# Kernel tuning notes

Measured on AMD Instinct MI355X. Metric: run time of the kernel, lower is better.

## Reference

```python
import jax, jax.numpy as jnp
import numpy as np

DIM = 576
NUM_HEADS = 1
HEAD_DIM = DIM // NUM_HEADS
SCALE = HEAD_DIM ** -0.5


def layer_norm(x, w, b, eps=1e-5):
    mu = jnp.mean(x, axis=-1, keepdims=True)
    var = jnp.var(x, axis=-1, keepdims=True)
    return (x - mu) * jax.lax.rsqrt(var + eps) * w + b


def setup_inputs() -> dict:
    key = jax.random.key(0)
    ks = jax.random.split(key, 10)
    B, N, C = 8, 2048, DIM
    s = C ** -0.5
    return {
        "x": jax.random.normal(ks[0], (B, N, C), jnp.float32),
        "y": jax.random.normal(ks[1], (B, N, C), jnp.float32),
        "Wq": jax.random.normal(ks[2], (C, C), jnp.float32) * s,
        "Wk": jax.random.normal(ks[3], (C, C), jnp.float32) * s,
        "Wv": jax.random.normal(ks[4], (C, C), jnp.float32) * s,
        "Wp": jax.random.normal(ks[5], (C, C), jnp.float32) * s,
        "bp": jnp.zeros((C,), jnp.float32),
        "gx": jnp.ones((C,), jnp.float32), "bx": jnp.zeros((C,), jnp.float32),
        "gy": jnp.ones((C,), jnp.float32), "by": jnp.zeros((C,), jnp.float32),
        "gz": jnp.ones((C,), jnp.float32), "bz": jnp.zeros((C,), jnp.float32),
    }


def reference(x, y, Wq, Wk, Wv, Wp, bp, gx, bx, gy, by, gz, bz):
    B, N, C = x.shape
    H, D = NUM_HEADS, HEAD_DIM
    xn = layer_norm(x, gx, bx)
    yn = layer_norm(y, gy, by)
    # torch Linear: out = in @ W^T
    q = (yn @ Wq.T).reshape(B, N, H, D).transpose(0, 2, 1, 3)  # [B,H,N,D]
    k = (xn @ Wk.T).reshape(B, N, H, D).transpose(0, 2, 1, 3)
    v = (xn @ Wv.T).reshape(B, N, H, D).transpose(0, 2, 1, 3)
    attn = jax.nn.sigmoid(jnp.einsum("bhnd,bhmd->bhnm", q, k) * SCALE)
    out = jnp.einsum("bhnm,bhmd->bhnd", attn, v).transpose(0, 2, 1, 3).reshape(B, N, C)
    out = out @ Wp.T + bp
    out = out + xn  # residual with normalized x
    return layer_norm(out, gz, bz)
```

## Files before the change

kernel.cpp:

```cpp
#include <hip/hip_runtime.h>

typedef __bf16 bfrag __attribute__((ext_vector_type(8)));
typedef float f32x4 __attribute__((ext_vector_type(4)));

__device__ __forceinline__ unsigned short f2bf(float f) {
    unsigned int u = __float_as_uint(f);
    unsigned int r = (u + 0x7fffu + ((u >> 16) & 1u)) >> 16;
    return (unsigned short)r;
}
__device__ __forceinline__ float bf2f(unsigned short h) {
    return __uint_as_float(((unsigned int)h) << 16);
}

__device__ __forceinline__ void gll16(const unsigned short* g, unsigned short* l) {
    __builtin_amdgcn_global_load_lds(
        (const __attribute__((address_space(1))) unsigned int*)g,
        (__attribute__((address_space(3))) unsigned int*)l, 16, 0, 0);
}

__device__ __forceinline__ float fsigmoid(float v) {
    return __builtin_amdgcn_rcpf(1.0f + __expf(-v));
}

__device__ __forceinline__ int swz(int r, int kc) {
    return (r >> 3) * 512 + (((r & 7) * 8 + (kc ^ (r & 7))) * 8);
}

template<int BM, int BN, int WR, int WC, int EPI, int TM, int TN, int N, int K>
__global__ __launch_bounds__(256) void gemm_nt(
    const unsigned short* __restrict__ A, const unsigned short* __restrict__ B,
    unsigned short* __restrict__ Cb,
    const unsigned short* __restrict__ R, const float* __restrict__ bias,
    float scale, size_t sAz, size_t sBz, size_t sCz)
{
    constexpr int BK = 64;
    constexpr int WTM = BM / (WR * 16);
    constexpr int WTN = BN / (WC * 16);
    constexpr int NA = BM / 32, NB = BN / 32;
    __shared__ unsigned short sA[BM * BK];
    __shared__ unsigned short sB[BN * BK];

    const int id  = blockIdx.x;
    const int j   = id >> 3;
    const int s   = (id & 7) + 8 * (j / TN);
    const int bn0 = (j % TN) * BN;
    const int bm0 = (s % TM) * BM;
    const int z   = s / TM;

    A += (size_t)z * sAz;
    B += (size_t)z * sBz;

    const int tid  = threadIdx.x;
    const int w    = tid >> 6;
    const int lane = tid & 63;
    const int wm = w / WC;
    const int wn = w % WC;
    const int rl  = lane >> 3;
    const int kcs = (lane & 7) ^ rl;
    const int mrow = lane & 15;
    const int kgrp = lane >> 4;

    const unsigned short* pA[NA];
    const unsigned short* pB[NB];
    #pragma unroll
    for (int i = 0; i < NA; ++i) {
        int wc = w * NA + i;
        pA[i] = A + (size_t)(bm0 + wc * 8 + rl) * K + kcs * 8;
    }
    #pragma unroll
    for (int i = 0; i < NB; ++i) {
        int wc = w * NB + i;
        pB[i] = B + (size_t)(bn0 + wc * 8 + rl) * K + kcs * 8;
    }

    f32x4 acc[WTM][WTN] = {};

    for (int k0 = 0; k0 < K; k0 += BK) {
        #pragma unroll
        for (int i = 0; i < NA; ++i) {
            gll16(pA[i], &sA[(w * NA + i) * 512 + lane * 8]);
            pA[i] += BK;
        }
        #pragma unroll
        for (int i = 0; i < NB; ++i) {
            gll16(pB[i], &sB[(w * NB + i) * 512 + lane * 8]);
            pB[i] += BK;
        }
        __syncthreads();

        #pragma unroll
        for (int kh = 0; kh < 2; ++kh) {
            bfrag af[WTM], bfr[WTN];
            #pragma unroll
            for (int mt = 0; mt < WTM; ++mt)
                af[mt] = *(const bfrag*)&sA[swz(wm * WTM * 16 + mt * 16 + mrow, kh * 4 + kgrp)];
            #pragma unroll
            for (int nt = 0; nt < WTN; ++nt)
                bfr[nt] = *(const bfrag*)&sB[swz(wn * WTN * 16 + nt * 16 + mrow, kh * 4 + kgrp)];
            #pragma unroll
            for (int mt = 0; mt < WTM; ++mt)
                #pragma unroll
                for (int nt = 0; nt < WTN; ++nt)
                    acc[mt][nt] = __builtin_amdgcn_mfma_f32_16x16x32_bf16(af[mt], bfr[nt], acc[mt][nt], 0, 0, 0);
        }
        __syncthreads();
    }

    #pragma unroll
    for (int mt = 0; mt < WTM; ++mt) {
        #pragma unroll
        for (int nt = 0; nt < WTN; ++nt) {
            int grow0 = bm0 + wm * WTM * 16 + mt * 16 + kgrp * 4;
            int gcol  = bn0 + wn * WTN * 16 + nt * 16 + mrow;
            #pragma unroll
            for (int r = 0; r < 4; ++r) {
                float v = acc[mt][nt][r];
                size_t off = (size_t)z * sCz + (size_t)(grow0 + r) * N + gcol;
                if (EPI == 0) {
                    Cb[off] = f2bf(v * scale);
                } else if (EPI == 1) {
                    Cb[off] = f2bf(fsigmoid(v));
                } else {
                    Cb[off] = f2bf(v + bias[gcol] + bf2f(R[off]));
                }
            }
        }
    }
}

__global__ __launch_bounds__(256) void qkv_proj(
    const unsigned short* __restrict__ xn, const unsigned short* __restrict__ yn,
    const unsigned short* __restrict__ W,
    unsigned short* __restrict__ qk,
    unsigned short* __restrict__ vt,
    float scale)
{
    constexpr int BM = 128, BN = 64, BK = 64;
    constexpr int WTM = 4, WTN = 2;
    constexpr int NA = 4, NB = 2;
    __shared__ unsigned short sA[BM * BK];
    __shared__ unsigned short sB[BN * BK];

    const int id  = blockIdx.x;
    const int j   = id >> 3;
    const int s   = (id & 7) + 8 * (j / 9);
    const int bn0 = (j % 9) * BN;
    const int bm0 = (s % 128) * BM;
    const int z   = s / 128;

    const unsigned short* A = (z == 0) ? yn : xn;
    const unsigned short* B = W + (size_t)z * 576 * 576;
    const float sc = (z == 0) ? scale : 1.0f;

    const int tid  = threadIdx.x;
    const int w    = tid >> 6;
    const int lane = tid & 63;
    const int wm = w >> 1;
    const int wn = w & 1;
    const int rl  = lane >> 3;
    const int kcs = (lane & 7) ^ rl;
    const int mrow = lane & 15;
    const int kgrp = lane >> 4;

    const unsigned short* pA[NA];
    const unsigned short* pB[NB];
    #pragma unroll
    for (int i = 0; i < NA; ++i) {
        int wc = w * NA + i;
        pA[i] = A + (size_t)(bm0 + wc * 8 + rl) * 576 + kcs * 8;
    }
    #pragma unroll
    for (int i = 0; i < NB; ++i) {
        int wc = w * NB + i;
        pB[i] = B + (size_t)(bn0 + wc * 8 + rl) * 576 + kcs * 8;
    }

    f32x4 acc[WTM][WTN] = {};

    for (int k0 = 0; k0 < 576; k0 += BK) {
        #pragma unroll
        for (int i = 0; i < NA; ++i) {
            gll16(pA[i], &sA[(w * NA + i) * 512 + lane * 8]);
            pA[i] += BK;
        }
        #pragma unroll
        for (int i = 0; i < NB; ++i) {
            gll16(pB[i], &sB[(w * NB + i) * 512 + lane * 8]);
            pB[i] += BK;
        }
        __syncthreads();

        #pragma unroll
        for (int kh = 0; kh < 2; ++kh) {
            bfrag af[WTM], bfr[WTN];
            #pragma unroll
            for (int mt = 0; mt < WTM; ++mt)
                af[mt] = *(const bfrag*)&sA[swz(wm * WTM * 16 + mt * 16 + mrow, kh * 4 + kgrp)];
            #pragma unroll
            for (int nt = 0; nt < WTN; ++nt)
                bfr[nt] = *(const bfrag*)&sB[swz(wn * WTN * 16 + nt * 16 + mrow, kh * 4 + kgrp)];
            #pragma unroll
            for (int mt = 0; mt < WTM; ++mt)
                #pragma unroll
                for (int nt = 0; nt < WTN; ++nt)
                    acc[mt][nt] = __builtin_amdgcn_mfma_f32_16x16x32_bf16(af[mt], bfr[nt], acc[mt][nt], 0, 0, 0);
        }
        __syncthreads();
    }

    #pragma unroll
    for (int mt = 0; mt < WTM; ++mt) {
        #pragma unroll
        for (int nt = 0; nt < WTN; ++nt) {
            int grow0 = bm0 + wm * WTM * 16 + mt * 16 + kgrp * 4;
            int gcol  = bn0 + wn * WTN * 16 + nt * 16 + mrow;
            if (z == 2) {
                ushort4 o;
                o.x = f2bf(acc[mt][nt][0]);
                o.y = f2bf(acc[mt][nt][1]);
                o.z = f2bf(acc[mt][nt][2]);
                o.w = f2bf(acc[mt][nt][3]);
                size_t dst = (((size_t)(grow0 >> 11) * 576 + gcol) << 11) + (grow0 & 2047);
                *(ushort4*)(vt + dst) = o;
            } else {
                unsigned short* C = qk + (size_t)z * 16384 * 576;
                #pragma unroll
                for (int r = 0; r < 4; ++r)
                    C[(size_t)(grow0 + r) * 576 + gcol] = f2bf(acc[mt][nt][r] * sc);
            }
        }
    }
}

__global__ __launch_bounds__(256) void ln_pair(
    const float* __restrict__ x, const float* __restrict__ gx, const float* __restrict__ bx,
    unsigned short* __restrict__ xn,
    const float* __restrict__ y, const float* __restrict__ gy, const float* __restrict__ by,
    unsigned short* __restrict__ yn)
{
    const float* src = blockIdx.y ? y : x;
    const float* g   = blockIdx.y ? gy : gx;
    const float* bb  = blockIdx.y ? by : bx;
    unsigned short* o = blockIdx.y ? yn : xn;

    const int row  = blockIdx.x * 4 + (threadIdx.x >> 6);
    const int lane = threadIdx.x & 63;
    const float* xr = src + (size_t)row * 576;
    float vals[9];
    float s = 0.f, ss = 0.f;
    #pragma unroll
    for (int i = 0; i < 9; ++i) {
        float v = xr[lane + i * 64];
        vals[i] = v; s += v; ss += v * v;
    }
    #pragma unroll
    for (int off = 32; off > 0; off >>= 1) {
        s  += __shfl_xor(s, off, 64);
        ss += __shfl_xor(ss, off, 64);
    }
    float mean = s * (1.0f / 576.0f);
    float var  = ss * (1.0f / 576.0f) - mean * mean;
    float rstd = rsqrtf(var + 1e-5f);
    #pragma unroll
    for (int i = 0; i < 9; ++i) {
        int c = lane + i * 64;
        o[(size_t)row * 576 + c] = f2bf((vals[i] - mean) * rstd * g[c] + bb[c]);
    }
}

__global__ __launch_bounds__(256) void ln_final(
    const unsigned short* __restrict__ x, const float* __restrict__ g,
    const float* __restrict__ bb, float* __restrict__ outp)
{
    const int row  = blockIdx.x * 4 + (threadIdx.x >> 6);
    const int lane = threadIdx.x & 63;
    const unsigned short* xr = x + (size_t)row * 576;
    float vals[9];
    float s = 0.f, ss = 0.f;
    #pragma unroll
    for (int i = 0; i < 9; ++i) {
        float v = bf2f(xr[lane + i * 64]);
        vals[i] = v; s += v; ss += v * v;
    }
    #pragma unroll
    for (int off = 32; off > 0; off >>= 1) {
        s  += __shfl_xor(s, off, 64);
        ss += __shfl_xor(ss, off, 64);
    }
    float mean = s * (1.0f / 576.0f);
    float var  = ss * (1.0f / 576.0f) - mean * mean;
    float rstd = rsqrtf(var + 1e-5f);
    #pragma unroll
    for (int i = 0; i < 9; ++i) {
        int c = lane + i * 64;
        outp[(size_t)row * 576 + c] = (vals[i] - mean) * rstd * g[c] + bb[c];
    }
}

__global__ __launch_bounds__(256) void cvt4w(
    const float* __restrict__ s0, const float* __restrict__ s1,
    const float* __restrict__ s2, const float* __restrict__ s3,
    unsigned short* __restrict__ dst)
{
    const float* srcs[4] = {s0, s1, s2, s3};
    const float* src = srcs[blockIdx.y];
    unsigned short* d = dst + (size_t)blockIdx.y * 576 * 576;
    int i = (blockIdx.x * 256 + threadIdx.x) * 4;
    float4 f = *(const float4*)(src + i);
    ushort4 o;
    o.x = f2bf(f.x); o.y = f2bf(f.y); o.z = f2bf(f.z); o.w = f2bf(f.w);
    *(ushort4*)(d + i) = o;
}

extern "C" void kernel_launch(void* const* d_in, const int* in_sizes, int n_in,
                              void* d_out, int out_size, void* d_ws, size_t ws_size,
                              hipStream_t stream)
{
    const float* x  = (const float*)d_in[0];
    const float* y  = (const float*)d_in[1];
    const float* Wq = (const float*)d_in[2];
    const float* Wk = (const float*)d_in[3];
    const float* Wv = (const float*)d_in[4];
    const float* Wp = (const float*)d_in[5];
    const float* bp = (const float*)d_in[6];
    const float* gx = (const float*)d_in[7];
    const float* bx = (const float*)d_in[8];
    const float* gy = (const float*)d_in[9];
    const float* by = (const float*)d_in[10];
    const float* gz = (const float*)d_in[11];
    const float* bz = (const float*)d_in[12];

    constexpr size_t WB = 576 * 576 * 2;
    constexpr size_t XB = 16384ull * 576 * 2;
    constexpr size_t TOK = (size_t)2048 * 576;
    constexpr size_t SB  = (size_t)2048 * 2048;

    char* w = (char*)d_ws;
    unsigned short* wq = (unsigned short*)(w);
    unsigned short* wp = (unsigned short*)(w + 3 * WB);
    unsigned short* xn = (unsigned short*)(w + 4 * WB);
    unsigned short* yn = (unsigned short*)(w + 4 * WB + XB);
    unsigned short* q  = (unsigned short*)(w + 4 * WB + 2 * XB);
    unsigned short* k  = (unsigned short*)(w + 4 * WB + 3 * XB);
    unsigned short* vt = (unsigned short*)(w + 4 * WB + 4 * XB);
    unsigned short* S  = (unsigned short*)(w + 4 * WB + 5 * XB);
    unsigned short* attno = yn;
    unsigned short* T = q;

    cvt4w<<<dim3(324, 4), 256, 0, stream>>>(Wq, Wk, Wv, Wp, wq);

    ln_pair<<<dim3(4096, 2), 256, 0, stream>>>(x, gx, bx, xn, y, gy, by, yn);

    const float SCALE = 0.041666666666666664f;
    qkv_proj<<<3456, 256, 0, stream>>>(xn, yn, wq, q, vt, SCALE);

    gemm_nt<128, 128, 2, 2, 1, 16, 16, 2048, 576><<<2048, 256, 0, stream>>>(
        q, k, S, nullptr, nullptr, 1.0f, TOK, TOK, SB);
    gemm_nt<128, 64, 2, 2, 0, 16, 9, 576, 2048><<<1152, 256, 0, stream>>>(
        S, vt, attno, nullptr, nullptr, 1.0f, SB, TOK, TOK);

    gemm_nt<128, 64, 2, 2, 2, 128, 9, 576, 576><<<1152, 256, 0, stream>>>(
        attno, wp, T, xn, bp, 1.0f, 0, 0, 0);
    ln_final<<<4096, 256, 0, stream>>>(T, gz, bz, (float*)d_out);
}
```

Measured before the change: 321.3 us.

## Replace LDS-staged QK^T GEMM with direct global-to-register MFMA kernel

The Q·K^T sigmoid GEMM no longer goes through the generic LDS-tiled gemm_nt path. It now uses a dedicated kernel in which each wave loads its bf16 MFMA fragments straight from global memory into registers, double-buffered across K chunks, with no shared memory and no barriers. The kernel relies on L2 to absorb the re-reads of Q and K tiles across waves. In exchange it removes LDS traffic and synchronisation, but uses strided 16-byte global loads that are poorly coalesced and more sensitive to latency.

```diff
diff --git a/kernel.cpp b/kernel.cpp
--- a/kernel.cpp
+++ b/kernel.cpp
@@ -24,6 +24,83 @@
 
 __device__ __forceinline__ int swz(int r, int kc) {
     return (r >> 3) * 512 + (((r & 7) * 8 + (kc ^ (r & 7))) * 8);
+}
+
+__global__ __launch_bounds__(256) void sgemm_l2(
+    const unsigned short* __restrict__ q, const unsigned short* __restrict__ k,
+    unsigned short* __restrict__ S)
+{
+    constexpr size_t TOK = (size_t)2048 * 576;
+    const int id  = blockIdx.x;
+    const int j   = id >> 3;
+    const int s   = (id & 7) + 8 * (j >> 4);
+    const int bn0 = (j & 15) * 128;
+    const int bm0 = (s & 15) * 128;
+    const int z   = s >> 4;
+
+    const unsigned short* A = q + (size_t)z * TOK;
+    const unsigned short* B = k + (size_t)z * TOK;
+
+    const int tid  = threadIdx.x;
+    const int w    = tid >> 6;
+    const int lane = tid & 63;
+    const int wm = w >> 1;
+    const int wn = w & 1;
+    const int mrow = lane & 15;
+    const int kgrp = lane >> 4;
+
+    const unsigned short* pA[4];
+    const unsigned short* pB[4];
+    #pragma unroll
+    for (int t = 0; t < 4; ++t) {
+        pA[t] = A + (size_t)(bm0 + wm * 64 + t * 16 + mrow) * 576 + kgrp * 8;
+        pB[t] = B + (size_t)(bn0 + wn * 64 + t * 16 + mrow) * 576 + kgrp * 8;
+    }
+
+    f32x4 acc[4][4] = {};
+    bfrag a0[4], b0[4], a1[4], b1[4];
+
+    #pragma unroll
+    for (int t = 0; t < 4; ++t) { a0[t] = *(const bfrag*)pA[t]; b0[t] = *(const bfrag*)pB[t]; }
+
+    #pragma unroll
+    for (int kc = 0; kc < 18; kc += 2) {
+        #pragma unroll
+        for (int t = 0; t < 4; ++t) {
+            a1[t] = *(const bfrag*)(pA[t] + (kc + 1) * 32);
+            b1[t] = *(const bfrag*)(pB[t] + (kc + 1) * 32);
+        }
+        #pragma unroll
+        for (int mt = 0; mt < 4; ++mt)
+            #pragma unroll
+            for (int nt = 0; nt < 4; ++nt)
+                acc[mt][nt] = __builtin_amdgcn_mfma_f32_16x16x32_bf16(a0[mt], b0[nt], acc[mt][nt], 0, 0, 0);
+        if (kc + 2 < 18) {
+            #pragma unroll
+            for (int t = 0; t < 4; ++t) {
+                a0[t] = *(const bfrag*)(pA[t] + (kc + 2) * 32);
+                b0[t] = *(const bfrag*)(pB[t] + (kc + 2) * 32);
+            }
+        }
+        #pragma unroll
+        for (int mt = 0; mt < 4; ++mt)
+            #pragma unroll
+            for (int nt = 0; nt < 4; ++nt)
+                acc[mt][nt] = __builtin_amdgcn_mfma_f32_16x16x32_bf16(a1[mt], b1[nt], acc[mt][nt], 0, 0, 0);
+    }
+
+    unsigned short* Sz = S + (size_t)z * 2048 * 2048;
+    #pragma unroll
+    for (int mt = 0; mt < 4; ++mt) {
+        #pragma unroll
+        for (int nt = 0; nt < 4; ++nt) {
+            int grow0 = bm0 + wm * 64 + mt * 16 + kgrp * 4;
+            int gcol  = bn0 + wn * 64 + nt * 16 + mrow;
+            #pragma unroll
+            for (int r = 0; r < 4; ++r)
+                Sz[(size_t)(grow0 + r) * 2048 + gcol] = f2bf(fsigmoid(acc[mt][nt][r]));
+        }
+    }
 }
 
 template<int BM, int BN, int WR, int WC, int EPI, int TM, int TN, int N, int K>
@@ -118,8 +195,6 @@
                 size_t off = (size_t)z * sCz + (size_t)(grow0 + r) * N + gcol;
                 if (EPI == 0) {
                     Cb[off] = f2bf(v * scale);
-                } else if (EPI == 1) {
-                    Cb[off] = f2bf(fsigmoid(v));
                 } else {
                     Cb[off] = f2bf(v + bias[gcol] + bf2f(R[off]));
                 }
@@ -354,8 +429,8 @@
     const float SCALE = 0.041666666666666664f;
     qkv_proj<<<3456, 256, 0, stream>>>(xn, yn, wq, q, vt, SCALE);
 
-    gemm_nt<128, 128, 2, 2, 1, 16, 16, 2048, 576><<<2048, 256, 0, stream>>>(
-        q, k, S, nullptr, nullptr, 1.0f, TOK, TOK, SB);
+    sgemm_l2<<<2048, 256, 0, stream>>>(q, k, S);
+
     gemm_nt<128, 64, 2, 2, 0, 16, 9, 576, 2048><<<1152, 256, 0, stream>>>(
         S, vt, attno, nullptr, nullptr, 1.0f, SB, TOK, TOK);
 
```

Result: slower. 419.1 us (+30.4%).
